# Kernel tuning notes

Hardware: AMD Instinct MI355X
Metric: run time of the kernel (lower is better)

## Reference

```python
import jax, jax.numpy as jnp
import numpy as np

N_NODES = 100000
N_EDGES = 1600000
IN_DIM = 128
OUT_DIM = 64


def setup_inputs() -> dict:
    key = jax.random.key(0)
    k1, k2, k3, k4 = jax.random.split(key, 4)
    h = jax.random.normal(k1, (N_NODES, IN_DIM), dtype=jnp.float32)
    W = jax.random.normal(k2, (OUT_DIM, IN_DIM), dtype=jnp.float32) * (1.0 / np.sqrt(IN_DIM))
    a_w = jax.random.normal(k3, (1, 2 * OUT_DIM), dtype=jnp.float32) * (1.0 / np.sqrt(2 * OUT_DIM))
    edge_index = jax.random.randint(k4, (2, N_EDGES), 0, N_NODES, dtype=jnp.int64 if jax.config.jax_enable_x64 else jnp.int32)
    return {"h": h, "W": W, "a_w": a_w, "edge_index": edge_index}


def reference(h, W, a_w, edge_index):
    # Wh: [N, out_dim]  (Linear without bias: x @ W.T)
    Wh = h @ W.T
    src, dst = edge_index[0], edge_index[1]
    # per-edge concat [Wh[src], Wh[dst]] -> [E, 2*out_dim]
    e = jnp.concatenate([Wh[src], Wh[dst]], axis=-1)
    # attention logits: [E]
    alpha = jax.nn.leaky_relu(e @ a_w.T, negative_slope=0.2)[:, 0]
    # global-max-stabilized exp (matches the torch code exactly)
    alpha_exp = jnp.exp(alpha - jnp.max(alpha))
    # segment softmax denominator over destination nodes: [N]
    alpha_sum = jax.ops.segment_sum(alpha_exp, dst, num_segments=N_NODES)
    alpha_norm = alpha_exp / (alpha_sum[dst] + 1e-9)
    # weighted scatter-add aggregation: [N, out_dim]
    out = jax.ops.segment_sum(alpha_norm[:, None] * Wh[src], dst, num_segments=N_NODES)
    return (jax.nn.elu(out), alpha_norm)
```

## Files before the change

### kernel.cpp

```cpp
#include <hip/hip_runtime.h>
#include <math.h>

#define N_NODES 100000
#define N_EDGES 1600000
#define IN_DIM 128
#define OUT_DIM 64

#define BSHIFT 9
#define BSIZE  (1 << BSHIFT)
#define NB     ((N_NODES + BSIZE - 1) >> BSHIFT)
#define EDGES_PER_BLK 2048
#define NBLK   ((N_EDGES + EDGES_PER_BLK - 1) / EDGES_PER_BLK)
#define SCANA_LEN (NB * NBLK)
#define SCANA_ITEMS 2048
#define SCANA_NB ((SCANA_LEN + SCANA_ITEMS - 1) / SCANA_ITEMS)

typedef short short8 __attribute__((ext_vector_type(8)));
typedef float f32x4 __attribute__((ext_vector_type(4)));
typedef float f32x2 __attribute__((ext_vector_type(2)));
typedef int   i32x4 __attribute__((ext_vector_type(4)));

__device__ __forceinline__ unsigned short f2bf(float x) {
    unsigned int u = __float_as_uint(x);
    return (unsigned short)((u + 0x7FFFu + ((u >> 16) & 1u)) >> 16);
}
__device__ __forceinline__ short8 pack_bf16x8(float4 p, float4 q) {
    short8 r;
    r[0] = (short)f2bf(p.x); r[1] = (short)f2bf(p.y);
    r[2] = (short)f2bf(p.z); r[3] = (short)f2bf(p.w);
    r[4] = (short)f2bf(q.x); r[5] = (short)f2bf(q.y);
    r[6] = (short)f2bf(q.z); r[7] = (short)f2bf(q.w);
    return r;
}
__device__ __forceinline__ void pk_fma(f32x2& d, f32x2 a, f32x2 b) {
    asm("v_pk_fma_f32 %0, %1, %2, %0" : "+v"(d) : "v"(a), "v"(b));
}

__global__ __launch_bounds__(256) void k_histA(const int* __restrict__ dst,
                                               int* __restrict__ hist_t,
                                               const float* __restrict__ W,
                                               const float* __restrict__ a_w,
                                               float* __restrict__ w1,
                                               float* __restrict__ w2) {
    __shared__ int lhist[NB];
    const int tid = threadIdx.x;
    const int blk = blockIdx.x;
    if (blk == 0 && tid < IN_DIM) {
        float r1 = 0.f, r2 = 0.f;
        #pragma unroll 8
        for (int dd = 0; dd < OUT_DIM; ++dd) {
            float wv = W[dd * IN_DIM + tid];
            r1 = fmaf(a_w[dd], wv, r1);
            r2 = fmaf(a_w[OUT_DIM + dd], wv, r2);
        }
        w1[tid] = r1; w2[tid] = r2;
    }
    if (tid < NB) lhist[tid] = 0;
    __syncthreads();
    const int e0 = blk * EDGES_PER_BLK;
    #pragma unroll
    for (int j = 0; j < 2; ++j) {
        int e = e0 + (j * 256 + tid) * 4;
        if (e < N_EDGES) {
            int4 d4 = *(const int4*)(dst + e);
            atomicAdd(&lhist[d4.x >> BSHIFT], 1);
            atomicAdd(&lhist[d4.y >> BSHIFT], 1);
            atomicAdd(&lhist[d4.z >> BSHIFT], 1);
            atomicAdd(&lhist[d4.w >> BSHIFT], 1);
        }
    }
    __syncthreads();
    if (tid < NB) hist_t[tid * NBLK + blk] = lhist[tid];
}

__global__ __launch_bounds__(256) void k_wh(const float* __restrict__ h,
                                            const float* __restrict__ W,
                                            const float* __restrict__ w1,
                                            const float* __restrict__ w2,
                                            unsigned short* __restrict__ Wh16,
                                            float* __restrict__ s1,
                                            float* __restrict__ s2) {
    const int tid = threadIdx.x;
    const int wv = tid >> 6;
    const int l  = tid & 63;
    const int g  = l >> 4;
    const int lm = l & 15;
    const int node0 = blockIdx.x * 64 + wv * 16;
    const int row = node0 + lm;
    const int rowc = (row < N_NODES) ? row : (N_NODES - 1);
    const float* hrow = h + (size_t)rowc * IN_DIM;

    short8 afrag[4];
    float sp1 = 0.f, sp2 = 0.f;
    #pragma unroll
    for (int kt = 0; kt < 4; ++kt) {
        const int k0 = kt * 32 + g * 8;
        float4 p = *(const float4*)(hrow + k0);
        float4 q = *(const float4*)(hrow + k0 + 4);
        float4 u1 = *(const float4*)(w1 + k0);
        float4 v1 = *(const float4*)(w1 + k0 + 4);
        float4 u2 = *(const float4*)(w2 + k0);
        float4 v2 = *(const float4*)(w2 + k0 + 4);
        sp1 += p.x*u1.x + p.y*u1.y + p.z*u1.z + p.w*u1.w
             + q.x*v1.x + q.y*v1.y + q.z*v1.z + q.w*v1.w;
        sp2 += p.x*u2.x + p.y*u2.y + p.z*u2.z + p.w*u2.w
             + q.x*v2.x + q.y*v2.y + q.z*v2.z + q.w*v2.w;
        afrag[kt] = pack_bf16x8(p, q);
    }
    sp1 += __shfl_xor(sp1, 16, 64); sp1 += __shfl_xor(sp1, 32, 64);
    sp2 += __shfl_xor(sp2, 16, 64); sp2 += __shfl_xor(sp2, 32, 64);
    if (l < 16 && row < N_NODES) { s1[row] = sp1; s2[row] = sp2; }

    f32x4 acc[4] = {f32x4{0,0,0,0}, f32x4{0,0,0,0}, f32x4{0,0,0,0}, f32x4{0,0,0,0}};
    #pragma unroll
    for (int nt = 0; nt < 4; ++nt) {
        #pragma unroll
        for (int kt = 0; kt < 4; ++kt) {
            const float* wr = W + (size_t)(nt * 16 + lm) * IN_DIM + kt * 32 + g * 8;
            float4 p = *(const float4*)wr;
            float4 q = *(const float4*)(wr + 4);
            short8 bfrag = pack_bf16x8(p, q);
            acc[nt] = __builtin_amdgcn_mfma_f32_16x16x32_bf16(afrag[kt], bfrag, acc[nt], 0, 0, 0);
        }
    }
    #pragma unroll
    for (int nt = 0; nt < 4; ++nt) {
        #pragma unroll
        for (int r = 0; r < 4; ++r) {
            int nodo = node0 + g * 4 + r;
            if (nodo < N_NODES)
                Wh16[(size_t)nodo * OUT_DIM + nt * 16 + lm] = f2bf(acc[nt][r]);
        }
    }
}

__global__ __launch_bounds__(256) void k_scanA_part(const int* __restrict__ in,
                                                    int* __restrict__ bsum) {
    __shared__ int wsum[4];
    const int tid = threadIdx.x;
    const int base = blockIdx.x * SCANA_ITEMS + tid * 8;
    int s = 0;
    if (base + 7 < SCANA_LEN) {
        int4 a = *(const int4*)(in + base);
        int4 b = *(const int4*)(in + base + 4);
        s = a.x + a.y + a.z + a.w + b.x + b.y + b.z + b.w;
    } else {
        for (int j = 0; j < 8; ++j)
            if (base + j < SCANA_LEN) s += in[base + j];
    }
    #pragma unroll
    for (int off = 32; off > 0; off >>= 1) s += __shfl_xor(s, off, 64);
    if ((tid & 63) == 0) wsum[tid >> 6] = s;
    __syncthreads();
    if (tid == 0) bsum[blockIdx.x] = wsum[0] + wsum[1] + wsum[2] + wsum[3];
}

__global__ __launch_bounds__(256) void k_scanA_final(const int* __restrict__ in,
                                                     const int* __restrict__ bsum,
                                                     int* __restrict__ outscan) {
    __shared__ int sb[256];
    __shared__ int wtot[4];
    const int tid = threadIdx.x;
    const int lane = tid & 63;
    const int wid = tid >> 6;
    sb[tid] = (tid < SCANA_NB) ? bsum[tid] : 0;
    __syncthreads();
    #pragma unroll
    for (int off = 1; off < 256; off <<= 1) {
        int u = (tid >= off) ? sb[tid - off] : 0;
        __syncthreads();
        sb[tid] += u;
        __syncthreads();
    }
    const int blockbase = (blockIdx.x > 0) ? sb[blockIdx.x - 1] : 0;
    const int base = blockIdx.x * SCANA_ITEMS + tid * 8;
    int c[8];
    if (base + 7 < SCANA_LEN) {
        int4 a = *(const int4*)(in + base);
        int4 b = *(const int4*)(in + base + 4);
        c[0]=a.x; c[1]=a.y; c[2]=a.z; c[3]=a.w;
        c[4]=b.x; c[5]=b.y; c[6]=b.z; c[7]=b.w;
    } else {
        #pragma unroll
        for (int j = 0; j < 8; ++j)
            c[j] = (base + j < SCANA_LEN) ? in[base + j] : 0;
    }
    int tot = 0;
    #pragma unroll
    for (int j = 0; j < 8; ++j) tot += c[j];
    int inc = tot;
    #pragma unroll
    for (int off = 1; off < 64; off <<= 1) {
        int u = __shfl_up(inc, off, 64);
        if (lane >= off) inc += u;
    }
    if (lane == 63) wtot[wid] = inc;
    __syncthreads();
    int wbase = 0;
    #pragma unroll
    for (int w = 0; w < 4; ++w) wbase += (w < wid) ? wtot[w] : 0;
    int run = blockbase + wbase + (inc - tot);
    #pragma unroll
    for (int j = 0; j < 8; ++j) {
        int i = base + j;
        if (i < SCANA_LEN) { outscan[i] = run; run += c[j]; }
    }
}

__global__ __launch_bounds__(256) void k_binA(const int* __restrict__ ei,
                                              const float* __restrict__ s1,
                                              const float* __restrict__ s2,
                                              const int* __restrict__ flat_scan,
                                              int2* __restrict__ brec,
                                              float* __restrict__ ae_orig) {
    __shared__ int lbase[NB];
    __shared__ int lcur[NB];
    const int tid = threadIdx.x;
    const int blk = blockIdx.x;
    if (tid < NB) { lbase[tid] = flat_scan[tid * NBLK + blk]; lcur[tid] = 0; }
    __syncthreads();
    const int e0 = blk * EDGES_PER_BLK;
    #pragma unroll
    for (int j = 0; j < 2; ++j) {
        int e = e0 + (j * 256 + tid) * 4;
        if (e >= N_EDGES) continue;
        int4 s4 = *(const int4*)(ei + e);
        int4 d4 = *(const int4*)(ei + N_EDGES + e);
        f32x4 aev;
        #pragma unroll
        for (int q = 0; q < 4; ++q) {
            int src = ((const int*)&s4)[q];
            int dst = ((const int*)&d4)[q];
            float a = s1[src] + s2[dst];
            a = (a > 0.f) ? a : 0.2f * a;
            float ae = expf(a);
            aev[q] = ae;
            int b = dst >> BSHIFT;
            int r = atomicAdd(&lcur[b], 1);
            brec[lbase[b] + r] = make_int2(src | ((dst & (BSIZE - 1)) << 17),
                                           __float_as_int(ae));
        }
        __builtin_nontemporal_store(aev, (f32x4*)(ae_orig + e));
    }
}

__global__ __launch_bounds__(1024) void k_fine(const int2* __restrict__ brec,
                                               const int* __restrict__ flat_scan,
                                               int* __restrict__ offsets,
                                               int2* __restrict__ sa_sorted,
                                               float* __restrict__ inv_tab) {
    __shared__ int lhist[BSIZE];
    __shared__ int lofs[BSIZE];
    __shared__ int lcur[BSIZE];
    __shared__ float lsum[BSIZE];
    __shared__ int wsum[4];
    const int tid = threadIdx.x;
    const int b = blockIdx.x;
    const int base = flat_scan[b * NBLK];
    const int endp = (b + 1 < NB) ? flat_scan[(b + 1) * NBLK] : N_EDGES;
    const int cnt = endp - base;
    if (tid < BSIZE) { lhist[tid] = 0; lsum[tid] = 0.f; }
    __syncthreads();
    for (int i = tid; i < cnt; i += 1024)
        atomicAdd(&lhist[(unsigned)brec[base + i].x >> 17], 1);
    __syncthreads();
    if (tid < 256) {
        const int lane = tid & 63;
        int c0 = lhist[2 * tid], c1 = lhist[2 * tid + 1];
        int s = c0 + c1;
        int inc = s;
        #pragma unroll
        for (int off = 1; off < 64; off <<= 1) {
            int u = __shfl_up(inc, off, 64);
            if (lane >= off) inc += u;
        }
        if (lane == 63) wsum[tid >> 6] = inc;
        lofs[2 * tid] = inc - s;
        lofs[2 * tid + 1] = c0;
    }
    __syncthreads();
    if (tid < 256) {
        const int wid = tid >> 6;
        int wb = 0;
        #pragma unroll
        for (int w = 0; w < 4; ++w) wb += (w < wid) ? wsum[w] : 0;
        int ex = lofs[2 * tid] + wb;
        int c0 = lofs[2 * tid + 1];
        lofs[2 * tid] = ex; lofs[2 * tid + 1] = ex + c0;
        lcur[2 * tid] = ex; lcur[2 * tid + 1] = ex + c0;
    }
    __syncthreads();
    const int dst0 = b << BSHIFT;
    if (tid < BSIZE) {
        int node = dst0 + tid;
        if (node < N_NODES) offsets[node] = base + lofs[tid];
    }
    if (b == NB - 1 && tid == 0) offsets[N_NODES] = N_EDGES;
    for (int i = tid; i < cnt; i += 1024) {
        int2 rec = brec[base + i];
        int dstl = (unsigned)rec.x >> 17;
        float ae = __int_as_float(rec.y);
        int pos = base + atomicAdd(&lcur[dstl], 1);
        sa_sorted[pos] = make_int2(rec.x & 0x1FFFF, rec.y);
        atomicAdd(&lsum[dstl], ae);
    }
    __syncthreads();
    if (tid < BSIZE) {
        int node = dst0 + tid;
        if (node < N_NODES) inv_tab[node] = 1.f / (lsum[tid] + 1e-9f);
    }
}

__global__ __launch_bounds__(256) void k_agg(const int2* __restrict__ sa_sorted,
                                             const int* __restrict__ offsets,
                                             const unsigned short* __restrict__ Wh16,
                                             const float* __restrict__ inv_tab,
                                             float* __restrict__ out) {
    const int gid = blockIdx.x * 256 + threadIdx.x;
    const int node = gid >> 6;
    const int l = gid & 63;
    if (node >= N_NODES) return;
    const int g = l >> 3;
    const int o = l & 7;
    const int beg = offsets[node];
    const int end = offsets[node + 1];
    f32x2 acc2[4] = {f32x2{0,0}, f32x2{0,0}, f32x2{0,0}, f32x2{0,0}};
    int i = beg;
    int2 pA, pB;
    bool have = (i + 16 <= end);
    if (have) { pA = sa_sorted[i + g]; pB = sa_sorted[i + 8 + g]; }
    while (have) {
        const int4 rA = *(const int4*)(Wh16 + ((size_t)pA.x << 6) + (o << 3));
        const int4 rB = *(const int4*)(Wh16 + ((size_t)pB.x << 6) + (o << 3));
        const float aeA = __int_as_float(pA.y);
        const float aeB = __int_as_float(pB.y);
        const int inext = i + 16;
        have = (inext + 16 <= end);
        if (have) { pA = sa_sorted[inext + g]; pB = sa_sorted[inext + 8 + g]; }
        i = inext;
        f32x2 a2A = {aeA, aeA}, a2B = {aeB, aeB};
        #pragma unroll
        for (int q = 0; q < 4; ++q) {
            int v = ((const int*)&rA)[q];
            f32x2 f = { __uint_as_float((unsigned)v << 16),
                        __uint_as_float((unsigned)v & 0xFFFF0000u) };
            pk_fma(acc2[q], f, a2A);
        }
        #pragma unroll
        for (int q = 0; q < 4; ++q) {
            int v = ((const int*)&rB)[q];
            f32x2 f = { __uint_as_float((unsigned)v << 16),
                        __uint_as_float((unsigned)v & 0xFFFF0000u) };
            pk_fma(acc2[q], f, a2B);
        }
    }
    for (; i < end; i += 8) {
        int idx = i + g;
        int2 p = (idx < end) ? sa_sorted[idx] : make_int2(0, 0);
        const int4 r = *(const int4*)(Wh16 + ((size_t)p.x << 6) + (o << 3));
        float ae = __int_as_float(p.y);
        f32x2 a2 = {ae, ae};
        #pragma unroll
        for (int q = 0; q < 4; ++q) {
            int v = ((const int*)&r)[q];
            f32x2 f = { __uint_as_float((unsigned)v << 16),
                        __uint_as_float((unsigned)v & 0xFFFF0000u) };
            pk_fma(acc2[q], f, a2);
        }
    }
    #pragma unroll
    for (int m = 8; m <= 32; m <<= 1) {
        #pragma unroll
        for (int q = 0; q < 4; ++q) {
            acc2[q].x += __shfl_xor(acc2[q].x, m, 64);
            acc2[q].y += __shfl_xor(acc2[q].y, m, 64);
        }
    }
    if (g == 0) {
        const float inv = inv_tab[node];
        float e[8];
        #pragma unroll
        for (int q = 0; q < 4; ++q) {
            float x0 = acc2[q].x * inv;
            float x1 = acc2[q].y * inv;
            e[2*q]   = (x0 > 0.f) ? x0 : expf(x0) - 1.f;
            e[2*q+1] = (x1 > 0.f) ? x1 : expf(x1) - 1.f;
        }
        float* orow = out + (size_t)node * OUT_DIM + o * 8;
        *(float4*)orow = make_float4(e[0], e[1], e[2], e[3]);
        *(float4*)(orow + 4) = make_float4(e[4], e[5], e[6], e[7]);
    }
}

__global__ __launch_bounds__(256) void k_norm(const int* __restrict__ dst_arr,
                                              const float* __restrict__ ae_orig,
                                              const float* __restrict__ inv_tab,
                                              float* __restrict__ alpha_norm) {
    int t = blockIdx.x * 256 + threadIdx.x;
    if (t >= N_EDGES / 4) return;
    i32x4 d4 = __builtin_nontemporal_load((const i32x4*)dst_arr + t);
    f32x4 a4 = __builtin_nontemporal_load((const f32x4*)ae_orig + t);
    f32x4 r;
    r.x = a4.x * inv_tab[d4.x];
    r.y = a4.y * inv_tab[d4.y];
    r.z = a4.z * inv_tab[d4.z];
    r.w = a4.w * inv_tab[d4.w];
    __builtin_nontemporal_store(r, (f32x4*)alpha_norm + t);
}

extern "C" void kernel_launch(void* const* d_in, const int* in_sizes, int n_in,
                              void* d_out, int out_size, void* d_ws, size_t ws_size,
                              hipStream_t stream) {
    const float* h   = (const float*)d_in[0];
    const float* W   = (const float*)d_in[1];
    const float* a_w = (const float*)d_in[2];
    const int*   ei  = (const int*)d_in[3];

    float* out        = (float*)d_out;
    float* alpha_norm = out + (size_t)N_NODES * OUT_DIM;

    char* ws = (char*)d_ws;
    int2* brec      = (int2*)ws;            ws += (size_t)N_EDGES * 8;
    int2* sa_sorted = (int2*)ws;            ws += (size_t)N_EDGES * 8;
    unsigned short* Wh16 = (unsigned short*)ws;  ws += (size_t)N_NODES * OUT_DIM * 2;
    float* ae_orig  = (float*)ws;           ws += (size_t)N_EDGES * 4;
    float* s1       = (float*)ws;           ws += (size_t)N_NODES * 4;
    float* s2       = (float*)ws;           ws += (size_t)N_NODES * 4;
    int*   hist_t   = (int*)ws;             ws += (size_t)SCANA_LEN * 4;
    int*   flat_scan= (int*)ws;             ws += (size_t)SCANA_LEN * 4;
    int*   bsum     = (int*)ws;             ws += (size_t)SCANA_NB * 4;
    int*   offsets  = (int*)ws;             ws += (size_t)(N_NODES + 1) * 4;
    float* inv_tab  = (float*)ws;           ws += (size_t)N_NODES * 4;
    float* w1       = (float*)ws;           ws += (size_t)IN_DIM * 4;
    float* w2       = (float*)ws;           ws += (size_t)IN_DIM * 4;

    k_histA<<<NBLK, 256, 0, stream>>>(ei + N_EDGES, hist_t, W, a_w, w1, w2);
    k_wh<<<(N_NODES + 63) / 64, 256, 0, stream>>>(h, W, w1, w2, Wh16, s1, s2);
    k_scanA_part<<<SCANA_NB, 256, 0, stream>>>(hist_t, bsum);
    k_scanA_final<<<SCANA_NB, 256, 0, stream>>>(hist_t, bsum, flat_scan);
    k_binA<<<NBLK, 256, 0, stream>>>(ei, s1, s2, flat_scan, brec, ae_orig);
    k_fine<<<NB, 1024, 0, stream>>>(brec, flat_scan, offsets, sa_sorted, inv_tab);
    k_agg<<<(N_NODES * 64 + 255) / 256, 256, 0, stream>>>(sa_sorted, offsets, Wh16,
                                                          inv_tab, out);
    k_norm<<<(N_EDGES / 4 + 255) / 256, 256, 0, stream>>>(ei + N_EDGES, ae_orig,
                                                          inv_tab, alpha_norm);
}
```

Measured before the change: 163.9 us.

## Merge histogram with Wh GEMM and aggregation with normalization into combined launches

The destination histogram and the Wh projection now run in one launch, split by block index. Each Wh block recomputes the folded attention vectors w1/w2 into shared memory, so the workspace copies and the dependency between the two kernels go away. The aggregation and alpha normalization kernels are likewise merged into one grid. The ELU output is now written as one float per lane instead of two float4 stores from a subset of lanes. This saves two launches and lets independent work overlap, at the cost of redundant w1/w2 computation in every Wh block and narrower output stores.

```diff
diff --git a/kernel.cpp b/kernel.cpp
--- a/kernel.cpp
+++ b/kernel.cpp
@@ -15,6 +15,10 @@
 #define SCANA_ITEMS 2048
 #define SCANA_NB ((SCANA_LEN + SCANA_ITEMS - 1) / SCANA_ITEMS)
 
+#define WH_BLOCKS ((N_NODES + 63) / 64)
+#define AGG_BLOCKS ((N_NODES * 64 + 255) / 256)
+#define NORM_BLOCKS ((N_EDGES / 4 + 255) / 256)
+
 typedef short short8 __attribute__((ext_vector_type(8)));
 typedef float f32x4 __attribute__((ext_vector_type(4)));
 typedef float f32x2 __attribute__((ext_vector_type(2)));
@@ -36,16 +40,39 @@
     asm("v_pk_fma_f32 %0, %1, %2, %0" : "+v"(d) : "v"(a), "v"(b));
 }
 
-__global__ __launch_bounds__(256) void k_histA(const int* __restrict__ dst,
-                                               int* __restrict__ hist_t,
-                                               const float* __restrict__ W,
-                                               const float* __restrict__ a_w,
-                                               float* __restrict__ w1,
-                                               float* __restrict__ w2) {
-    __shared__ int lhist[NB];
-    const int tid = threadIdx.x;
-    const int blk = blockIdx.x;
-    if (blk == 0 && tid < IN_DIM) {
+__global__ __launch_bounds__(256) void k_histwh(const int* __restrict__ dst,
+                                                int* __restrict__ hist_t,
+                                                const float* __restrict__ h,
+                                                const float* __restrict__ W,
+                                                const float* __restrict__ a_w,
+                                                unsigned short* __restrict__ Wh16,
+                                                float* __restrict__ s1,
+                                                float* __restrict__ s2) {
+    const int tid = threadIdx.x;
+    if (blockIdx.x < NBLK) {
+        __shared__ int lhist[NB];
+        const int blk = blockIdx.x;
+        if (tid < NB) lhist[tid] = 0;
+        __syncthreads();
+        const int e0 = blk * EDGES_PER_BLK;
+        #pragma unroll
+        for (int j = 0; j < 2; ++j) {
+            int e = e0 + (j * 256 + tid) * 4;
+            if (e < N_EDGES) {
+                int4 d4 = *(const int4*)(dst + e);
+                atomicAdd(&lhist[d4.x >> BSHIFT], 1);
+                atomicAdd(&lhist[d4.y >> BSHIFT], 1);
+                atomicAdd(&lhist[d4.z >> BSHIFT], 1);
+                atomicAdd(&lhist[d4.w >> BSHIFT], 1);
+            }
+        }
+        __syncthreads();
+        if (tid < NB) hist_t[tid * NBLK + blk] = lhist[tid];
+        return;
+    }
+    __shared__ float w1s[IN_DIM];
+    __shared__ float w2s[IN_DIM];
+    if (tid < IN_DIM) {
         float r1 = 0.f, r2 = 0.f;
         #pragma unroll 8
         for (int dd = 0; dd < OUT_DIM; ++dd) {
@@ -53,39 +80,14 @@
             r1 = fmaf(a_w[dd], wv, r1);
             r2 = fmaf(a_w[OUT_DIM + dd], wv, r2);
         }
-        w1[tid] = r1; w2[tid] = r2;
-    }
-    if (tid < NB) lhist[tid] = 0;
-    __syncthreads();
-    const int e0 = blk * EDGES_PER_BLK;
-    #pragma unroll
-    for (int j = 0; j < 2; ++j) {
-        int e = e0 + (j * 256 + tid) * 4;
-        if (e < N_EDGES) {
-            int4 d4 = *(const int4*)(dst + e);
-            atomicAdd(&lhist[d4.x >> BSHIFT], 1);
-            atomicAdd(&lhist[d4.y >> BSHIFT], 1);
-            atomicAdd(&lhist[d4.z >> BSHIFT], 1);
-            atomicAdd(&lhist[d4.w >> BSHIFT], 1);
-        }
-    }
-    __syncthreads();
-    if (tid < NB) hist_t[tid * NBLK + blk] = lhist[tid];
-}
-
-__global__ __launch_bounds__(256) void k_wh(const float* __restrict__ h,
-                                            const float* __restrict__ W,
-                                            const float* __restrict__ w1,
-                                            const float* __restrict__ w2,
-                                            unsigned short* __restrict__ Wh16,
-                                            float* __restrict__ s1,
-                                            float* __restrict__ s2) {
-    const int tid = threadIdx.x;
+        w1s[tid] = r1; w2s[tid] = r2;
+    }
+    __syncthreads();
     const int wv = tid >> 6;
     const int l  = tid & 63;
     const int g  = l >> 4;
     const int lm = l & 15;
-    const int node0 = blockIdx.x * 64 + wv * 16;
+    const int node0 = (blockIdx.x - NBLK) * 64 + wv * 16;
     const int row = node0 + lm;
     const int rowc = (row < N_NODES) ? row : (N_NODES - 1);
     const float* hrow = h + (size_t)rowc * IN_DIM;
@@ -97,10 +99,10 @@
         const int k0 = kt * 32 + g * 8;
         float4 p = *(const float4*)(hrow + k0);
         float4 q = *(const float4*)(hrow + k0 + 4);
-        float4 u1 = *(const float4*)(w1 + k0);
-        float4 v1 = *(const float4*)(w1 + k0 + 4);
-        float4 u2 = *(const float4*)(w2 + k0);
-        float4 v2 = *(const float4*)(w2 + k0 + 4);
+        float4 u1 = *(const float4*)(w1s + k0);
+        float4 v1 = *(const float4*)(w1s + k0 + 4);
+        float4 u2 = *(const float4*)(w2s + k0);
+        float4 v2 = *(const float4*)(w2s + k0 + 4);
         sp1 += p.x*u1.x + p.y*u1.y + p.z*u1.z + p.w*u1.w
              + q.x*v1.x + q.y*v1.y + q.z*v1.z + q.w*v1.w;
         sp2 += p.x*u2.x + p.y*u2.y + p.z*u2.z + p.w*u2.w
@@ -311,12 +313,29 @@
     }
 }
 
-__global__ __launch_bounds__(256) void k_agg(const int2* __restrict__ sa_sorted,
-                                             const int* __restrict__ offsets,
-                                             const unsigned short* __restrict__ Wh16,
-                                             const float* __restrict__ inv_tab,
-                                             float* __restrict__ out) {
-    const int gid = blockIdx.x * 256 + threadIdx.x;
+__global__ __launch_bounds__(256) void k_aggnorm(const int2* __restrict__ sa_sorted,
+                                                 const int* __restrict__ offsets,
+                                                 const unsigned short* __restrict__ Wh16,
+                                                 const float* __restrict__ inv_tab,
+                                                 float* __restrict__ out,
+                                                 const int* __restrict__ dst_arr,
+                                                 const float* __restrict__ ae_orig,
+                                                 float* __restrict__ alpha_norm) {
+    const int tid = threadIdx.x;
+    if (blockIdx.x >= AGG_BLOCKS) {
+        int t = (blockIdx.x - AGG_BLOCKS) * 256 + tid;
+        if (t >= N_EDGES / 4) return;
+        i32x4 d4 = __builtin_nontemporal_load((const i32x4*)dst_arr + t);
+        f32x4 a4 = __builtin_nontemporal_load((const f32x4*)ae_orig + t);
+        f32x4 r;
+        r.x = a4.x * inv_tab[d4.x];
+        r.y = a4.y * inv_tab[d4.y];
+        r.z = a4.z * inv_tab[d4.z];
+        r.w = a4.w * inv_tab[d4.w];
+        __builtin_nontemporal_store(r, (f32x4*)alpha_norm + t);
+        return;
+    }
+    const int gid = blockIdx.x * 256 + tid;
     const int node = gid >> 6;
     const int l = gid & 63;
     if (node >= N_NODES) return;
@@ -376,36 +395,13 @@
             acc2[q].y += __shfl_xor(acc2[q].y, m, 64);
         }
     }
-    if (g == 0) {
-        const float inv = inv_tab[node];
-        float e[8];
-        #pragma unroll
-        for (int q = 0; q < 4; ++q) {
-            float x0 = acc2[q].x * inv;
-            float x1 = acc2[q].y * inv;
-            e[2*q]   = (x0 > 0.f) ? x0 : expf(x0) - 1.f;
-            e[2*q+1] = (x1 > 0.f) ? x1 : expf(x1) - 1.f;
-        }
-        float* orow = out + (size_t)node * OUT_DIM + o * 8;
-        *(float4*)orow = make_float4(e[0], e[1], e[2], e[3]);
-        *(float4*)(orow + 4) = make_float4(e[4], e[5], e[6], e[7]);
-    }
-}
-
-__global__ __launch_bounds__(256) void k_norm(const int* __restrict__ dst_arr,
-                                              const float* __restrict__ ae_orig,
-                                              const float* __restrict__ inv_tab,
-                                              float* __restrict__ alpha_norm) {
-    int t = blockIdx.x * 256 + threadIdx.x;
-    if (t >= N_EDGES / 4) return;
-    i32x4 d4 = __builtin_nontemporal_load((const i32x4*)dst_arr + t);
-    f32x4 a4 = __builtin_nontemporal_load((const f32x4*)ae_orig + t);
-    f32x4 r;
-    r.x = a4.x * inv_tab[d4.x];
-    r.y = a4.y * inv_tab[d4.y];
-    r.z = a4.z * inv_tab[d4.z];
-    r.w = a4.w * inv_tab[d4.w];
-    __builtin_nontemporal_store(r, (f32x4*)alpha_norm + t);
+    const float inv = inv_tab[node];
+    const int q = g >> 1;
+    float vx = (q == 0) ? acc2[0].x : (q == 1) ? acc2[1].x : (q == 2) ? acc2[2].x : acc2[3].x;
+    float vy = (q == 0) ? acc2[0].y : (q == 1) ? acc2[1].y : (q == 2) ? acc2[2].y : acc2[3].y;
+    float x = ((g & 1) ? vy : vx) * inv;
+    x = (x > 0.f) ? x : expf(x) - 1.f;
+    out[(size_t)node * OUT_DIM + o * 8 + g] = x;
 }
 
 extern "C" void kernel_launch(void* const* d_in, const int* in_sizes, int n_in,
@@ -431,17 +427,15 @@
     int*   bsum     = (int*)ws;             ws += (size_t)SCANA_NB * 4;
     int*   offsets  = (int*)ws;             ws += (size_t)(N_NODES + 1) * 4;
     float* inv_tab  = (float*)ws;           ws += (size_t)N_NODES * 4;
-    float* w1       = (float*)ws;           ws += (size_t)IN_DIM * 4;
-    float* w2       = (float*)ws;           ws += (size_t)IN_DIM * 4;
-
-    k_histA<<<NBLK, 256, 0, stream>>>(ei + N_EDGES, hist_t, W, a_w, w1, w2);
-    k_wh<<<(N_NODES + 63) / 64, 256, 0, stream>>>(h, W, w1, w2, Wh16, s1, s2);
+
+    k_histwh<<<NBLK + WH_BLOCKS, 256, 0, stream>>>(ei + N_EDGES, hist_t,
+                                                   h, W, a_w, Wh16, s1, s2);
     k_scanA_part<<<SCANA_NB, 256, 0, stream>>>(hist_t, bsum);
     k_scanA_final<<<SCANA_NB, 256, 0, stream>>>(hist_t, bsum, flat_scan);
     k_binA<<<NBLK, 256, 0, stream>>>(ei, s1, s2, flat_scan, brec, ae_orig);
     k_fine<<<NB, 1024, 0, stream>>>(brec, flat_scan, offsets, sa_sorted, inv_tab);
-    k_agg<<<(N_NODES * 64 + 255) / 256, 256, 0, stream>>>(sa_sorted, offsets, Wh16,
-                                                          inv_tab, out);
-    k_norm<<<(N_EDGES / 4 + 255) / 256, 256, 0, stream>>>(ei + N_EDGES, ae_orig,
-                                                          inv_tab, alpha_norm);
-}
+    k_aggnorm<<<AGG_BLOCKS + NORM_BLOCKS, 256, 0, stream>>>(sa_sorted, offsets, Wh16,
+                                                            inv_tab, out,
+                                                            ei + N_EDGES, ae_orig,
+                                                            alpha_norm);
+}
```

New measurement: 141.8 us (median of 2 runs). 1.16x faster.
